# Optimization experiments

Hardware: AMD Instinct MI355X
Metric: run time of the kernel (lower is better)

## Reference

```python
import jax, jax.numpy as jnp
import numpy as np

N_TXN, N_CLI, N_E = 100000, 20000, 600000
D_TXN, D_CLI, H = 64, 32, 128


def setup_inputs() -> dict:
    key = jax.random.key(0)
    ks = jax.random.split(key, 24)
    s = 0.05
    inp = {
        'x_txn': jax.random.normal(ks[0], (N_TXN, D_TXN), jnp.float32),
        'x_client': jax.random.normal(ks[1], (N_CLI, D_CLI), jnp.float32),
        'ei_ct_src': jax.random.randint(ks[2], (N_E,), 0, N_CLI),
        'ei_ct_dst': jax.random.randint(ks[3], (N_E,), 0, N_TXN),
        'ei_tc_src': jax.random.randint(ks[4], (N_E,), 0, N_TXN),
        'ei_tc_dst': jax.random.randint(ks[5], (N_E,), 0, N_CLI),
        'W1_ct_l': jax.random.normal(ks[6], (D_CLI, H), jnp.float32) * s,
        'b1_ct': jnp.zeros((H,), jnp.float32),
        'W1_ct_r': jax.random.normal(ks[7], (D_TXN, H), jnp.float32) * s,
        'W1_tc_l': jax.random.normal(ks[8], (D_TXN, H), jnp.float32) * s,
        'b1_tc': jnp.zeros((H,), jnp.float32),
        'W1_tc_r': jax.random.normal(ks[9], (D_CLI, H), jnp.float32) * s,
        'W2_ct_l': jax.random.normal(ks[10], (H, H), jnp.float32) * s,
        'b2_ct': jnp.zeros((H,), jnp.float32),
        'W2_ct_r': jax.random.normal(ks[11], (H, H), jnp.float32) * s,
        'W2_tc_l': jax.random.normal(ks[12], (H, H), jnp.float32) * s,
        'b2_tc': jnp.zeros((H,), jnp.float32),
        'W2_tc_r': jax.random.normal(ks[13], (H, H), jnp.float32) * s,
        'Wd1': jax.random.normal(ks[14], (H, 64), jnp.float32) * s,
        'bd1': jnp.zeros((64,), jnp.float32),
        'Wd2': jax.random.normal(ks[15], (64, D_TXN), jnp.float32) * s,
        'bd2': jnp.zeros((D_TXN,), jnp.float32),
    }
    return inp


def _sage(x_src, x_dst, src, dst, Wl, bl, Wr, n_dst):
    # PyG SAGEConv: lin_l(mean_j x_src[j]) + lin_r(x_dst); lin_r has no bias.
    msg = x_src[src]                                             # [E, d_src]
    agg = jax.ops.segment_sum(msg, dst, num_segments=n_dst)     # [n_dst, d_src]
    cnt = jax.ops.segment_sum(jnp.ones((src.shape[0],), x_src.dtype), dst,
                              num_segments=n_dst)
    mean = agg / jnp.maximum(cnt, 1.0)[:, None]
    return mean @ Wl + bl + x_dst @ Wr


def reference(x_txn, x_client, ei_ct_src, ei_ct_dst, ei_tc_src, ei_tc_dst,
              W1_ct_l, b1_ct, W1_ct_r, W1_tc_l, b1_tc, W1_tc_r,
              W2_ct_l, b2_ct, W2_ct_r, W2_tc_l, b2_tc, W2_tc_r,
              Wd1, bd1, Wd2, bd2):
    # Layer 1 (hetero SAGEConv), then ReLU; dropout is identity in eval mode.
    h_txn = _sage(x_client, x_txn, ei_ct_src, ei_ct_dst, W1_ct_l, b1_ct, W1_ct_r, N_TXN)
    h_cli = _sage(x_txn, x_client, ei_tc_src, ei_tc_dst, W1_tc_l, b1_tc, W1_tc_r, N_CLI)
    h_txn = jax.nn.relu(h_txn)
    h_cli = jax.nn.relu(h_cli)
    # Layer 2
    z_txn = _sage(h_cli, h_txn, ei_ct_src, ei_ct_dst, W2_ct_l, b2_ct, W2_ct_r, N_TXN)
    z_cli = _sage(h_txn, h_cli, ei_tc_src, ei_tc_dst, W2_tc_l, b2_tc, W2_tc_r, N_CLI)
    # Decoder MLP on transaction embeddings
    recon = jax.nn.relu(z_txn @ Wd1 + bd1) @ Wd2 + bd2
    return (recon, z_txn, z_cli)
```

## Files before the change

### kernel.cpp

```cpp
#include <hip/hip_runtime.h>
#include <hip/hip_bf16.h>

typedef __hip_bfloat16 bf16;
typedef unsigned int uint;
typedef unsigned short ushort;
typedef __attribute__((ext_vector_type(8))) short short8;
typedef __attribute__((ext_vector_type(4))) float float4v;

__device__ __forceinline__ float lo2f(uint v) { return __uint_as_float(v << 16); }
__device__ __forceinline__ float hi2f(uint v) { return __uint_as_float(v & 0xffff0000u); }
__device__ __forceinline__ ushort f2bu(float v) {
  union { bf16 h; ushort u; } x;
  x.h = __float2bfloat16(v);
  return x.u;
}
__device__ __forceinline__ uint packbf2(float a, float b) {
  return (uint)f2bu(a) | ((uint)f2bu(b) << 16);
}

#define BSH 8
#define NBK_MAX 391

struct TJob { const float* wl; const float* wr; ushort* dst; int da, k, ncol, boff; };
struct TJobs { TJob j[6]; };

__global__ void transpose6_kernel(TJobs js) {
  int b = blockIdx.x;
  int jj = 0;
#pragma unroll
  for (int t = 1; t < 6; ++t)
    if (b >= js.j[t].boff) jj = t;
  const TJob J = js.j[jj];
  int i = (b - J.boff) * 256 + threadIdx.x;
  if (i >= J.k * J.ncol) return;
  int k = i / J.ncol, c = i - k * J.ncol;
  const float* srcp = (k < J.da) ? (J.wl + (long long)k * J.ncol)
                                 : (J.wr + (long long)(k - J.da) * J.ncol);
  J.dst[(long long)c * J.k + k] = f2bu(srcp[c]);
}

__global__ void bhist_kernel(const int* __restrict__ dA, int* __restrict__ cA, int nbkA,
                             const int* __restrict__ dB, int* __restrict__ cB, int nbkB,
                             int E, int chA) {
  __shared__ int h[NBK_MAX];
  int b = blockIdx.x;
  const int* dst; int* gc; int nbk;
  if (b < chA) { dst = dA; gc = cA; nbk = nbkA; }
  else         { b -= chA; dst = dB; gc = cB; nbk = nbkB; }
  for (int i = threadIdx.x; i < nbk; i += 256) h[i] = 0;
  __syncthreads();
  int e0 = b * 4096;
  for (int j = 0; j < 16; ++j) {
    int e = e0 + j * 256 + threadIdx.x;
    if (e < E) {
      uint B = (uint)dst[e] >> BSH;
      if (B < (uint)nbk) atomicAdd(&h[B], 1);
    }
  }
  __syncthreads();
  for (int i = threadIdx.x; i < nbk; i += 256)
    if (h[i]) atomicAdd(&gc[i], h[i]);
}

__global__ void bscan_kernel(const int* __restrict__ cA, int* __restrict__ oA,
                             int* __restrict__ uA, int nbkA,
                             const int* __restrict__ cB, int* __restrict__ oB,
                             int* __restrict__ uB, int nbkB) {
  __shared__ int s[512];
  const int* cnt; int* off; int* cur; int nbk;
  if (blockIdx.x == 0) { cnt = cA; off = oA; cur = uA; nbk = nbkA; }
  else                 { cnt = cB; off = oB; cur = uB; nbk = nbkB; }
  int t = threadIdx.x;
  int v = (t < nbk) ? cnt[t] : 0;
  s[t] = v;
  __syncthreads();
  for (int o = 1; o < 512; o <<= 1) {
    int x = (t >= o) ? s[t - o] : 0;
    __syncthreads();
    s[t] += x;
    __syncthreads();
  }
  if (t < nbk) { int ex = s[t] - v; off[t] = ex; cur[t] = ex; }
  if (t == nbk - 1) off[nbk] = s[t];
}

__global__ void multisplit_kernel(const int* __restrict__ sA, const int* __restrict__ dA,
                                  int* __restrict__ uA, uint2* __restrict__ seA, int nbkA,
                                  const int* __restrict__ sB, const int* __restrict__ dB,
                                  int* __restrict__ uB, uint2* __restrict__ seB, int nbkB,
                                  int E, int chA) {
  __shared__ int cnt[NBK_MAX];
  __shared__ int base[NBK_MAX];
  int b = blockIdx.x;
  const int *src, *dst; int* gcur; uint2* se; int nbk;
  if (b < chA) { src = sA; dst = dA; gcur = uA; se = seA; nbk = nbkA; }
  else         { b -= chA; src = sB; dst = dB; gcur = uB; se = seB; nbk = nbkB; }
  for (int i = threadIdx.x; i < nbk; i += 256) cnt[i] = 0;
  __syncthreads();
  int e0 = b * 4096;
  int mys[16], myd[16], myb[16], myr[16];
#pragma unroll
  for (int j = 0; j < 16; ++j) {
    int e = e0 + j * 256 + threadIdx.x;
    int s = 0, d = 0, bb = -1, r = 0;
    if (e < E) {
      s = src[e]; d = dst[e];
      uint B = (uint)d >> BSH;
      if (B < (uint)nbk) { bb = (int)B; r = atomicAdd(&cnt[bb], 1); }
    }
    mys[j] = s; myd[j] = d; myb[j] = bb; myr[j] = r;
  }
  __syncthreads();
  for (int i = threadIdx.x; i < nbk; i += 256) {
    int c = cnt[i];
    base[i] = c ? atomicAdd(&gcur[i], c) : 0;
  }
  __syncthreads();
#pragma unroll
  for (int j = 0; j < 16; ++j) {
    if (myb[j] >= 0) {
      uint2 v; v.x = (uint)mys[j]; v.y = (uint)myd[j];
      se[base[myb[j]] + myr[j]] = v;
    }
  }
}

__global__ void csr_fine_kernel(const uint2* __restrict__ seA, const int* __restrict__ boA,
                                int* __restrict__ offA, int* __restrict__ csrA, int nA, int nbkA,
                                const uint2* __restrict__ seB, const int* __restrict__ boB,
                                int* __restrict__ offB, int* __restrict__ csrB, int nB) {
  __shared__ int s[256];
  __shared__ int cur[256];
  int b = blockIdx.x;
  const uint2* se; const int* bo; int* off; int* csr; int n;
  if (b < nbkA) { se = seA; bo = boA; off = offA; csr = csrA; n = nA; }
  else          { b -= nbkA; se = seB; bo = boB; off = offB; csr = csrB; n = nB; }
  int t = threadIdx.x;
  int ebeg = bo[b], eend = bo[b + 1];
  cur[t] = 0;
  __syncthreads();
  for (int i = ebeg + t; i < eend; i += 256)
    atomicAdd(&cur[se[i].y & 255], 1);
  __syncthreads();
  int v = cur[t];
  s[t] = v;
  __syncthreads();
  for (int o = 1; o < 256; o <<= 1) {
    int x = (t >= o) ? s[t - o] : 0;
    __syncthreads();
    s[t] += x;
    __syncthreads();
  }
  int excl = s[t] - v;
  int node = b * 256 + t;
  if (node < n) off[node] = ebeg + excl;
  if (node == n - 1) off[n] = ebeg + excl + v;
  cur[t] = excl;
  __syncthreads();
  for (int i = ebeg + t; i < eend; i += 256) {
    uint2 e = se[i];
    int pos = ebeg + atomicAdd(&cur[e.y & 255], 1);
    csr[pos] = (int)e.x;
  }
}

__device__ __forceinline__ void acc8(float* a, uint4 v) {
  a[0] += lo2f(v.x); a[1] += hi2f(v.x);
  a[2] += lo2f(v.y); a[3] += hi2f(v.y);
  a[4] += lo2f(v.z); a[5] += hi2f(v.z);
  a[6] += lo2f(v.w); a[7] += hi2f(v.w);
}
__device__ __forceinline__ void acc4(float* a, float4 v) {
  a[0] += v.x; a[1] += v.y; a[2] += v.z; a[3] += v.w;
}

template <int D, bool XBF>
__device__ __forceinline__ void pull_worker(
    const int* __restrict__ off, const int* __restrict__ csr,
    const void* __restrict__ x, bf16* __restrict__ mean, int n, int nsrc,
    int blk0) {
  constexpr int EPL = XBF ? 8 : 4;
  constexpr int LPR = D / EPL;
  constexpr int PAR = 64 / LPR;
  int node = ((int)blockIdx.x - blk0) * 4 + (threadIdx.x >> 6);
  if (node >= n) return;
  int lane = threadIdx.x & 63;
  int h = lane / LPR, col = lane % LPR;
  int beg = off[node], deg = off[node + 1] - beg;
  float inv = 1.0f / fmaxf((float)deg, 1.0f);
  float a[EPL];
#pragma unroll
  for (int e = 0; e < EPL; ++e) a[e] = 0.f;

  int i = h;
  for (; i + 3 * PAR < deg; i += 4 * PAR) {
    int s0 = csr[beg + i];
    int s1 = csr[beg + i + PAR];
    int s2 = csr[beg + i + 2 * PAR];
    int s3 = csr[beg + i + 3 * PAR];
    s0 = ((unsigned)s0 < (unsigned)nsrc) ? s0 : 0;
    s1 = ((unsigned)s1 < (unsigned)nsrc) ? s1 : 0;
    s2 = ((unsigned)s2 < (unsigned)nsrc) ? s2 : 0;
    s3 = ((unsigned)s3 < (unsigned)nsrc) ? s3 : 0;
    if (XBF) {
      uint4 v0 = ((const uint4*)x)[(long long)s0 * LPR + col];
      uint4 v1 = ((const uint4*)x)[(long long)s1 * LPR + col];
      uint4 v2 = ((const uint4*)x)[(long long)s2 * LPR + col];
      uint4 v3 = ((const uint4*)x)[(long long)s3 * LPR + col];
      acc8(a, v0); acc8(a, v1); acc8(a, v2); acc8(a, v3);
    } else {
      float4 v0 = ((const float4*)x)[(long long)s0 * LPR + col];
      float4 v1 = ((const float4*)x)[(long long)s1 * LPR + col];
      float4 v2 = ((const float4*)x)[(long long)s2 * LPR + col];
      float4 v3 = ((const float4*)x)[(long long)s3 * LPR + col];
      acc4(a, v0); acc4(a, v1); acc4(a, v2); acc4(a, v3);
    }
  }
  for (; i < deg; i += PAR) {
    int s = csr[beg + i];
    s = ((unsigned)s < (unsigned)nsrc) ? s : 0;
    if (XBF) {
      uint4 v = ((const uint4*)x)[(long long)s * LPR + col];
      acc8(a, v);
    } else {
      float4 v = ((const float4*)x)[(long long)s * LPR + col];
      acc4(a, v);
    }
  }

#pragma unroll
  for (int m = LPR; m < 64; m <<= 1) {
#pragma unroll
    for (int e = 0; e < EPL; ++e) a[e] += __shfl_xor(a[e], m);
  }
  if (h == 0) {
    if (XBF) {
      uint4 o4;
      o4.x = packbf2(a[0] * inv, a[1] * inv);
      o4.y = packbf2(a[2] * inv, a[3] * inv);
      o4.z = packbf2(a[4] * inv, a[5] * inv);
      o4.w = packbf2(a[6] * inv, a[7] * inv);
      ((uint4*)mean)[(long long)node * LPR + col] = o4;
    } else {
      uint2 o2;
      o2.x = packbf2(a[0] * inv, a[1] * inv);
      o2.y = packbf2(a[2] * inv, a[3] * inv);
      ((uint2*)mean)[(long long)node * LPR + col] = o2;
    }
  }
}

template <int DA, bool XA, int DB, bool XB>
__global__ __launch_bounds__(256) void pull2_kernel(
    const int* __restrict__ offA, const int* __restrict__ csrA,
    const void* __restrict__ xA, bf16* __restrict__ meanA, int nA, int nsrcA,
    const int* __restrict__ offB, const int* __restrict__ csrB,
    const void* __restrict__ xB, bf16* __restrict__ meanB, int nB, int nsrcB,
    int nblkA) {
  if ((int)blockIdx.x < nblkA)
    pull_worker<DA, XA>(offA, csrA, xA, meanA, nA, nsrcA, 0);
  else
    pull_worker<DB, XB>(offB, csrB, xB, meanB, nB, nsrcB, nblkA);
}

#define AT_BF16 0
#define AT_F32  1
template <int KT, int NCT, int K0T, int A0T, int A1T, bool OUTF32, int MT>
__global__ __launch_bounds__(256, 2) void gemm_kernel(
    const void* __restrict__ A0, int lda0,
    const void* __restrict__ A1, int lda1,
    const ushort* __restrict__ Wt, const float* __restrict__ bias,
    void* __restrict__ C, long long cbase, int ldc, int n, int relu) {
  constexpr int K = KT * 32;
  int tid = threadIdx.x;
  int wave = tid >> 6, lane = tid & 63;
  int p = lane & 15, q = lane >> 4;
  int rowbase = blockIdx.x * (64 * MT) + wave * (16 * MT);

  int rcl[MT];
#pragma unroll
  for (int m = 0; m < MT; ++m) rcl[m] = min(rowbase + m * 16 + p, n - 1);

  float4v acc[MT][NCT];
#pragma unroll
  for (int m = 0; m < MT; ++m)
#pragma unroll
    for (int t = 0; t < NCT; ++t) acc[m][t] = (float4v){0.f, 0.f, 0.f, 0.f};

#pragma unroll
  for (int kt = 0; kt < KT; ++kt) {
    const bool seg0 = (kt < K0T);
    const void* ab = seg0 ? A0 : A1;
    const int lda = seg0 ? lda0 : lda1;
    const int kof = (seg0 ? kt : (kt - K0T)) * 32;
    const int at = seg0 ? A0T : A1T;
    short8 af[MT];
#pragma unroll
    for (int m = 0; m < MT; ++m) {
      long long base = (long long)rcl[m] * lda + kof + q * 8;
      if (at == AT_BF16) {
        af[m] = *(const short8*)((const bf16*)ab + base);
      } else {
        const float* fb = (const float*)ab + base;
        float4 a = *(const float4*)fb;
        float4 b = *(const float4*)(fb + 4);
        short8 r;
        r[0] = (short)f2bu(a.x); r[1] = (short)f2bu(a.y);
        r[2] = (short)f2bu(a.z); r[3] = (short)f2bu(a.w);
        r[4] = (short)f2bu(b.x); r[5] = (short)f2bu(b.y);
        r[6] = (short)f2bu(b.z); r[7] = (short)f2bu(b.w);
        af[m] = r;
      }
    }
#pragma unroll
    for (int t = 0; t < NCT; ++t) {
      int c = t * 16 + p;
      short8 bfr = *(const short8*)(Wt + (long long)c * K + kt * 32 + q * 8);
#pragma unroll
      for (int m = 0; m < MT; ++m)
        acc[m][t] = __builtin_amdgcn_mfma_f32_16x16x32_bf16(af[m], bfr, acc[m][t], 0, 0, 0);
    }
  }

#pragma unroll
  for (int m = 0; m < MT; ++m) {
#pragma unroll
    for (int t = 0; t < NCT; ++t) {
      int c = t * 16 + p;
      float bv = bias[c];
#pragma unroll
      for (int r = 0; r < 4; ++r) {
        int row = rowbase + m * 16 + q * 4 + r;
        if (row < n) {
          float v = acc[m][t][r] + bv;
          if (relu) v = fmaxf(v, 0.f);
          long long idx = cbase + (long long)row * ldc + c;
          if (OUTF32) ((float*)C)[idx] = v;
          else        ((bf16*)C)[idx] = __float2bfloat16(v);
        }
      }
    }
  }
}

__global__ __launch_bounds__(256, 2) void gemm_fused_dec_kernel(
    const bf16* __restrict__ A0,
    const bf16* __restrict__ A1,
    const ushort* __restrict__ W3,
    const float* __restrict__ b2,
    const ushort* __restrict__ W5,
    const float* __restrict__ bd1v,
    const ushort* __restrict__ W6,
    const float* __restrict__ bd2v,
    float* __restrict__ zout,
    float* __restrict__ recon,
    int n) {
  __shared__ __align__(16) char zls[65536];
  int tid = threadIdx.x;
  int wave = tid >> 6, lane = tid & 63;
  int p = lane & 15, q = lane >> 4;
  int rowbase = blockIdx.x * 256 + wave * 64;
  char* wls = zls + wave * 16384;
  const int sw = (p & 7) << 4;

  int rcl[4];
#pragma unroll
  for (int m = 0; m < 4; ++m) rcl[m] = min(rowbase + m * 16 + p, n - 1);

  float4v accz[4][8];
#pragma unroll
  for (int m = 0; m < 4; ++m)
#pragma unroll
    for (int t = 0; t < 8; ++t) accz[m][t] = (float4v){0.f, 0.f, 0.f, 0.f};

#pragma unroll
  for (int kt = 0; kt < 8; ++kt) {
    const bf16* ab = (kt < 4) ? A0 : A1;
    const int kof = (kt & 3) * 32;
    short8 af[4];
#pragma unroll
    for (int m = 0; m < 4; ++m)
      af[m] = *(const short8*)(ab + (long long)rcl[m] * 128 + kof + q * 8);
#pragma unroll
    for (int t = 0; t < 8; ++t) {
      short8 bfr = *(const short8*)(W3 + (long long)(t * 16 + p) * 256 + kt * 32 + q * 8);
#pragma unroll
      for (int m = 0; m < 4; ++m)
        accz[m][t] = __builtin_amdgcn_mfma_f32_16x16x32_bf16(bfr, af[m], accz[m][t], 0, 0, 0);
    }
  }

#pragma unroll
  for (int m = 0; m < 4; ++m) {
    int lr = m * 16 + p;
    int row = rowbase + lr;
#pragma unroll
    for (int t = 0; t < 8; ++t) {
      float4v bz = *(const float4v*)(b2 + t * 16 + q * 4);
      float4v v;
#pragma unroll
      for (int r = 0; r < 4; ++r) v[r] = accz[m][t][r] + bz[r];
      if (row < n)
        *(float4v*)(zout + (long long)row * 128 + t * 16 + q * 4) = v;
      uint2 u;
      u.x = packbf2(v[0], v[1]);
      u.y = packbf2(v[2], v[3]);
      *(uint2*)(wls + (((lr * 256 + t * 32 + q * 8)) ^ sw)) = u;
    }
  }
  __syncthreads();

  float4v accd[4][4];
#pragma unroll
  for (int m = 0; m < 4; ++m)
#pragma unroll
    for (int t = 0; t < 4; ++t) accd[m][t] = (float4v){0.f, 0.f, 0.f, 0.f};

#pragma unroll
  for (int kt2 = 0; kt2 < 4; ++kt2) {
    short8 zf[4];
#pragma unroll
    for (int m = 0; m < 4; ++m)
      zf[m] = *(const short8*)(wls + (((m * 16 + p) * 256 + kt2 * 64 + q * 16) ^ sw));
#pragma unroll
    for (int t2 = 0; t2 < 4; ++t2) {
      short8 wf = *(const short8*)(W5 + (long long)(t2 * 16 + p) * 128 + kt2 * 32 + q * 8);
#pragma unroll
      for (int m = 0; m < 4; ++m)
        accd[m][t2] = __builtin_amdgcn_mfma_f32_16x16x32_bf16(wf, zf[m], accd[m][t2], 0, 0, 0);
    }
  }
  __syncthreads();

#pragma unroll
  for (int m = 0; m < 4; ++m) {
    int lr = m * 16 + p;
#pragma unroll
    for (int t2 = 0; t2 < 4; ++t2) {
      float4v bb = *(const float4v*)(bd1v + t2 * 16 + q * 4);
      float4v v;
#pragma unroll
      for (int r = 0; r < 4; ++r) v[r] = fmaxf(accd[m][t2][r] + bb[r], 0.f);
      uint2 u;
      u.x = packbf2(v[0], v[1]);
      u.y = packbf2(v[2], v[3]);
      *(uint2*)(wls + (((lr * 128 + t2 * 32 + q * 8)) ^ sw)) = u;
    }
  }

  float4v accr[4][4];
#pragma unroll
  for (int m = 0; m < 4; ++m)
#pragma unroll
    for (int t = 0; t < 4; ++t) accr[m][t] = (float4v){0.f, 0.f, 0.f, 0.f};

#pragma unroll
  for (int kt3 = 0; kt3 < 2; ++kt3) {
    short8 df[4];
#pragma unroll
    for (int m = 0; m < 4; ++m)
      df[m] = *(const short8*)(wls + (((m * 16 + p) * 128 + kt3 * 64 + q * 16) ^ sw));
#pragma unroll
    for (int t3 = 0; t3 < 4; ++t3) {
      short8 wf = *(const short8*)(W6 + (long long)(t3 * 16 + p) * 64 + kt3 * 32 + q * 8);
#pragma unroll
      for (int m = 0; m < 4; ++m)
        accr[m][t3] = __builtin_amdgcn_mfma_f32_16x16x32_bf16(wf, df[m], accr[m][t3], 0, 0, 0);
    }
  }

#pragma unroll
  for (int m = 0; m < 4; ++m) {
    int row = rowbase + m * 16 + p;
    if (row < n) {
#pragma unroll
      for (int t3 = 0; t3 < 4; ++t3) {
        float4v bb = *(const float4v*)(bd2v + t3 * 16 + q * 4);
        float4v v;
#pragma unroll
        for (int r = 0; r < 4; ++r) v[r] = accr[m][t3][r] + bb[r];
        *(float4v*)(recon + (long long)row * 64 + t3 * 16 + q * 4) = v;
      }
    }
  }
}

extern "C" void kernel_launch(void* const* d_in, const int* in_sizes, int n_in,
                              void* d_out, int out_size, void* d_ws,
                              size_t ws_size, hipStream_t stream) {
  const float* x_txn = (const float*)d_in[0];
  const float* x_cli = (const float*)d_in[1];
  const int* ct_src = (const int*)d_in[2];
  const int* ct_dst = (const int*)d_in[3];
  const int* tc_src = (const int*)d_in[4];
  const int* tc_dst = (const int*)d_in[5];
  const float* W1ctl = (const float*)d_in[6];
  const float* b1ct  = (const float*)d_in[7];
  const float* W1ctr = (const float*)d_in[8];
  const float* W1tcl = (const float*)d_in[9];
  const float* b1tc  = (const float*)d_in[10];
  const float* W1tcr = (const float*)d_in[11];
  const float* W2ctl = (const float*)d_in[12];
  const float* b2ct  = (const float*)d_in[13];
  const float* W2ctr = (const float*)d_in[14];
  const float* W2tcl = (const float*)d_in[15];
  const float* b2tc  = (const float*)d_in[16];
  const float* W2tcr = (const float*)d_in[17];
  const float* Wd1   = (const float*)d_in[18];
  const float* bd1   = (const float*)d_in[19];
  const float* Wd2   = (const float*)d_in[20];
  const float* bd2   = (const float*)d_in[21];

  const int E = in_sizes[2];
  const int NT = 100000, NC = 20000;
  const int NBK_CT = (NT + 255) >> 8;
  const int NBK_TC = (NC + 255) >> 8;

  size_t o = 0;
  auto carve = [&](size_t bytes) {
    void* p = (char*)d_ws + o;
    o = (o + bytes + 255) & ~(size_t)255;
    return p;
  };
  int* bcnt_ct = (int*)carve((size_t)NBK_CT * 4);
  int* bcnt_tc = (int*)carve((size_t)NBK_TC * 4);
  size_t zero_bytes = o;
  int* boff_ct = (int*)carve((size_t)(NBK_CT + 1) * 4);
  int* boff_tc = (int*)carve((size_t)(NBK_TC + 1) * 4);
  int* bcur_ct = (int*)carve((size_t)NBK_CT * 4);
  int* bcur_tc = (int*)carve((size_t)NBK_TC * 4);
  uint2* se_ct = (uint2*)carve((size_t)E * 8);
  uint2* se_tc = (uint2*)carve((size_t)E * 8);
  int* off_ct = (int*)carve((size_t)(NT + 1) * 4);
  int* off_tc = (int*)carve((size_t)(NC + 1) * 4);
  int* csr_ct = (int*)carve((size_t)E * 4);
  int* csr_tc = (int*)carve((size_t)E * 4);
  ushort* Wt1 = (ushort*)carve((size_t)96 * 128 * 2);
  ushort* Wt2 = (ushort*)carve((size_t)96 * 128 * 2);
  ushort* Wt3 = (ushort*)carve((size_t)256 * 128 * 2);
  ushort* Wt4 = (ushort*)carve((size_t)256 * 128 * 2);
  ushort* Wt5 = (ushort*)carve((size_t)128 * 64 * 2);
  ushort* Wt6 = (ushort*)carve((size_t)64 * 64 * 2);
  bf16* mean1_ct = (bf16*)carve((size_t)NT * 32 * 2);
  bf16* mean1_tc = (bf16*)carve((size_t)NC * 64 * 2);
  bf16* h_txn    = (bf16*)carve((size_t)NT * 128 * 2);
  bf16* h_cli    = (bf16*)carve((size_t)NC * 128 * 2);
  bf16* mean2_ct = (bf16*)carve((size_t)NT * 128 * 2);
  bf16* mean2_tc = (bf16*)carve((size_t)NC * 128 * 2);
  (void)ws_size;

  hipMemsetAsync(d_ws, 0, zero_bytes, stream);

  const int tb = 256;
  const int CH = (E + 4095) / 4096;

  {
    TJobs js;
    auto blocks = [](int k, int ncol) { return (k * ncol + 255) / 256; };
    int boff = 0;
    auto setj = [&](int idx, const float* wl, const float* wr, ushort* dst,
                    int da, int k, int ncol) {
      js.j[idx] = TJob{wl, wr, dst, da, k, ncol, boff};
      boff += blocks(k, ncol);
    };
    setj(0, W1ctl, W1ctr, Wt1, 32, 96, 128);
    setj(1, W1tcl, W1tcr, Wt2, 64, 96, 128);
    setj(2, W2ctl, W2ctr, Wt3, 128, 256, 128);
    setj(3, W2tcl, W2tcr, Wt4, 128, 256, 128);
    setj(4, Wd1, Wd1, Wt5, 128, 128, 64);
    setj(5, Wd2, Wd2, Wt6, 64, 64, 64);
    transpose6_kernel<<<boff, tb, 0, stream>>>(js);
  }

  bhist_kernel<<<2 * CH, tb, 0, stream>>>(ct_dst, bcnt_ct, NBK_CT,
                                          tc_dst, bcnt_tc, NBK_TC, E, CH);
  bscan_kernel<<<2, 512, 0, stream>>>(bcnt_ct, boff_ct, bcur_ct, NBK_CT,
                                      bcnt_tc, boff_tc, bcur_tc, NBK_TC);
  multisplit_kernel<<<2 * CH, tb, 0, stream>>>(
      ct_src, ct_dst, bcur_ct, se_ct, NBK_CT,
      tc_src, tc_dst, bcur_tc, se_tc, NBK_TC, E, CH);
  csr_fine_kernel<<<NBK_CT + NBK_TC, tb, 0, stream>>>(
      se_ct, boff_ct, off_ct, csr_ct, NT, NBK_CT,
      se_tc, boff_tc, off_tc, csr_tc, NC);

  auto gbm = [](int n, int mt) { return (n + 64 * mt - 1) / (64 * mt); };
  const int pbA = (NT + 3) / 4, pbB = (NC + 3) / 4;

  pull2_kernel<32, false, 64, false><<<pbA + pbB, tb, 0, stream>>>(
      off_ct, csr_ct, x_cli, mean1_ct, NT, NC,
      off_tc, csr_tc, x_txn, mean1_tc, NC, NT, pbA);

  gemm_kernel<3, 8, 1, AT_BF16, AT_F32, false, 4><<<gbm(NT, 4), tb, 0, stream>>>(
      mean1_ct, 32, x_txn, 64, Wt1, b1ct, h_txn, 0, 128, NT, 1);
  gemm_kernel<3, 8, 2, AT_BF16, AT_F32, false, 1><<<gbm(NC, 1), tb, 0, stream>>>(
      mean1_tc, 64, x_cli, 32, Wt2, b1tc, h_cli, 0, 128, NC, 1);

  pull2_kernel<128, true, 128, true><<<pbA + pbB, tb, 0, stream>>>(
      off_ct, csr_ct, h_cli, mean2_ct, NT, NC,
      off_tc, csr_tc, h_txn, mean2_tc, NC, NT, pbA);

  float* out = (float*)d_out;
  const long long ztxn_base = (long long)NT * 64;
  const long long zcli_base = ztxn_base + (long long)NT * 128;

  gemm_fused_dec_kernel<<<gbm(NT, 4), tb, 0, stream>>>(
      mean2_ct, h_txn, Wt3, b2ct, Wt5, bd1, Wt6, bd2,
      out + ztxn_base, out, NT);

  gemm_kernel<8, 8, 4, AT_BF16, AT_BF16, true, 1><<<gbm(NC, 1), tb, 0, stream>>>(
      mean2_tc, 128, h_cli, 128, Wt4, b2tc, out, zcli_base, 128, NC, 0);
}
```

Baseline: 376.6 us.

## Fuse txn-side neighbor mean aggregation into both layer GEMM kernels via LDS

The client-to-transaction mean aggregation is moved into the GEMM kernels for both layers. Each wave gathers its 64 rows' neighbor sums into swizzled LDS and feeds them straight to MFMA, so the mean1_ct and mean2_ct intermediates are never written to or read back from global memory. The combined pull kernels become client-only pull kernels. The cost is that gather latency now sits inside GEMM blocks with lower occupancy, and the layer-1 kernel converts fp32 x_txn to bf16 on the fly.

```diff
diff --git a/kernel.cpp b/kernel.cpp
--- a/kernel.cpp
+++ b/kernel.cpp
@@ -250,17 +250,11 @@
   }
 }
 
-template <int DA, bool XA, int DB, bool XB>
-__global__ __launch_bounds__(256) void pull2_kernel(
-    const int* __restrict__ offA, const int* __restrict__ csrA,
-    const void* __restrict__ xA, bf16* __restrict__ meanA, int nA, int nsrcA,
-    const int* __restrict__ offB, const int* __restrict__ csrB,
-    const void* __restrict__ xB, bf16* __restrict__ meanB, int nB, int nsrcB,
-    int nblkA) {
-  if ((int)blockIdx.x < nblkA)
-    pull_worker<DA, XA>(offA, csrA, xA, meanA, nA, nsrcA, 0);
-  else
-    pull_worker<DB, XB>(offB, csrB, xB, meanB, nB, nsrcB, nblkA);
+template <int D, bool XBF>
+__global__ __launch_bounds__(256) void pull1_kernel(
+    const int* __restrict__ off, const int* __restrict__ csr,
+    const void* __restrict__ x, bf16* __restrict__ mean, int n, int nsrc) {
+  pull_worker<D, XBF>(off, csr, x, mean, n, nsrc, 0);
 }
 
 #define AT_BF16 0
@@ -343,8 +337,109 @@
   }
 }
 
+__global__ __launch_bounds__(256, 2) void gemm1a_fused_kernel(
+    const int* __restrict__ off, const int* __restrict__ csr,
+    const float* __restrict__ xg,
+    const float* __restrict__ A1,
+    const ushort* __restrict__ Wt,
+    const float* __restrict__ bias,
+    bf16* __restrict__ C,
+    int n, int nsrc) {
+  __shared__ __align__(16) char mls[16384];
+  int tid = threadIdx.x, wave = tid >> 6, lane = tid & 63;
+  int p = lane & 15, q = lane >> 4;
+  int rowbase = blockIdx.x * 256 + wave * 64;
+  char* wls = mls + wave * 4096;
+
+  {
+    int g = lane >> 3, li = lane & 7;
+    for (int it = 0; it < 8; ++it) {
+      int lr = it * 8 + g;
+      int node = min(rowbase + lr, n - 1);
+      int beg = off[node], deg = off[node + 1] - beg;
+      float inv = 1.0f / fmaxf((float)deg, 1.0f);
+      float4 a0 = {0.f, 0.f, 0.f, 0.f}, a1 = {0.f, 0.f, 0.f, 0.f};
+      int j = 0;
+      for (; j + 1 < deg; j += 2) {
+        int s0 = csr[beg + j], s1 = csr[beg + j + 1];
+        s0 = ((unsigned)s0 < (unsigned)nsrc) ? s0 : 0;
+        s1 = ((unsigned)s1 < (unsigned)nsrc) ? s1 : 0;
+        float4 v0 = ((const float4*)xg)[(long long)s0 * 8 + li];
+        float4 v1 = ((const float4*)xg)[(long long)s1 * 8 + li];
+        a0.x += v0.x; a0.y += v0.y; a0.z += v0.z; a0.w += v0.w;
+        a1.x += v1.x; a1.y += v1.y; a1.z += v1.z; a1.w += v1.w;
+      }
+      if (j < deg) {
+        int s0 = csr[beg + j];
+        s0 = ((unsigned)s0 < (unsigned)nsrc) ? s0 : 0;
+        float4 v0 = ((const float4*)xg)[(long long)s0 * 8 + li];
+        a0.x += v0.x; a0.y += v0.y; a0.z += v0.z; a0.w += v0.w;
+      }
+      uint2 u;
+      u.x = packbf2((a0.x + a1.x) * inv, (a0.y + a1.y) * inv);
+      u.y = packbf2((a0.z + a1.z) * inv, (a0.w + a1.w) * inv);
+      *(uint2*)(wls + ((lr * 64 + li * 8) ^ ((lr & 3) << 4))) = u;
+    }
+  }
+
+  int rcl[4];
+#pragma unroll
+  for (int m = 0; m < 4; ++m) rcl[m] = min(rowbase + m * 16 + p, n - 1);
+
+  float4v acc[4][8];
+#pragma unroll
+  for (int m = 0; m < 4; ++m)
+#pragma unroll
+    for (int t = 0; t < 8; ++t) acc[m][t] = (float4v){0.f, 0.f, 0.f, 0.f};
+
+  const int sw1 = (p & 3) << 4;
+#pragma unroll
+  for (int kt = 0; kt < 3; ++kt) {
+    short8 af[4];
+#pragma unroll
+    for (int m = 0; m < 4; ++m) {
+      if (kt == 0) {
+        af[m] = *(const short8*)(wls + ((((m * 16 + p) * 64) + q * 16) ^ sw1));
+      } else {
+        const float* fb = A1 + (long long)rcl[m] * 64 + (kt - 1) * 32 + q * 8;
+        float4 a = *(const float4*)fb;
+        float4 b = *(const float4*)(fb + 4);
+        short8 r;
+        r[0] = (short)f2bu(a.x); r[1] = (short)f2bu(a.y);
+        r[2] = (short)f2bu(a.z); r[3] = (short)f2bu(a.w);
+        r[4] = (short)f2bu(b.x); r[5] = (short)f2bu(b.y);
+        r[6] = (short)f2bu(b.z); r[7] = (short)f2bu(b.w);
+        af[m] = r;
+      }
+    }
+#pragma unroll
+    for (int t = 0; t < 8; ++t) {
+      short8 bfr = *(const short8*)(Wt + (long long)(t * 16 + p) * 96 + kt * 32 + q * 8);
+#pragma unroll
+      for (int m = 0; m < 4; ++m)
+        acc[m][t] = __builtin_amdgcn_mfma_f32_16x16x32_bf16(af[m], bfr, acc[m][t], 0, 0, 0);
+    }
+  }
+
+#pragma unroll
+  for (int m = 0; m < 4; ++m) {
+#pragma unroll
+    for (int t = 0; t < 8; ++t) {
+      int c = t * 16 + p;
+      float bv = bias[c];
+#pragma unroll
+      for (int r = 0; r < 4; ++r) {
+        int row = rowbase + m * 16 + q * 4 + r;
+        if (row < n)
+          C[(long long)row * 128 + c] = __float2bfloat16(fmaxf(acc[m][t][r] + bv, 0.f));
+      }
+    }
+  }
+}
+
 __global__ __launch_bounds__(256, 2) void gemm_fused_dec_kernel(
-    const bf16* __restrict__ A0,
+    const int* __restrict__ off, const int* __restrict__ csr,
+    const bf16* __restrict__ xg,
     const bf16* __restrict__ A1,
     const ushort* __restrict__ W3,
     const float* __restrict__ b2,
@@ -354,7 +449,7 @@
     const float* __restrict__ bd2v,
     float* __restrict__ zout,
     float* __restrict__ recon,
-    int n) {
+    int n, int nsrc) {
   __shared__ __align__(16) char zls[65536];
   int tid = threadIdx.x;
   int wave = tid >> 6, lane = tid & 63;
@@ -363,6 +458,40 @@
   char* wls = zls + wave * 16384;
   const int sw = (p & 7) << 4;
 
+  {
+    int g = lane >> 4, li = lane & 15;
+    for (int it = 0; it < 16; ++it) {
+      int lr = it * 4 + g;
+      int node = min(rowbase + lr, n - 1);
+      int beg = off[node], deg = off[node + 1] - beg;
+      float inv = 1.0f / fmaxf((float)deg, 1.0f);
+      float a0[8], a1[8];
+#pragma unroll
+      for (int e = 0; e < 8; ++e) { a0[e] = 0.f; a1[e] = 0.f; }
+      int j = 0;
+      for (; j + 1 < deg; j += 2) {
+        int s0 = csr[beg + j], s1 = csr[beg + j + 1];
+        s0 = ((unsigned)s0 < (unsigned)nsrc) ? s0 : 0;
+        s1 = ((unsigned)s1 < (unsigned)nsrc) ? s1 : 0;
+        uint4 v0 = ((const uint4*)xg)[(long long)s0 * 16 + li];
+        uint4 v1 = ((const uint4*)xg)[(long long)s1 * 16 + li];
+        acc8(a0, v0); acc8(a1, v1);
+      }
+      if (j < deg) {
+        int s0 = csr[beg + j];
+        s0 = ((unsigned)s0 < (unsigned)nsrc) ? s0 : 0;
+        uint4 v0 = ((const uint4*)xg)[(long long)s0 * 16 + li];
+        acc8(a0, v0);
+      }
+      uint4 u;
+      u.x = packbf2((a0[0] + a1[0]) * inv, (a0[1] + a1[1]) * inv);
+      u.y = packbf2((a0[2] + a1[2]) * inv, (a0[3] + a1[3]) * inv);
+      u.z = packbf2((a0[4] + a1[4]) * inv, (a0[5] + a1[5]) * inv);
+      u.w = packbf2((a0[6] + a1[6]) * inv, (a0[7] + a1[7]) * inv);
+      *(uint4*)(wls + ((lr * 256 + li * 16) ^ ((lr & 7) << 4))) = u;
+    }
+  }
+
   int rcl[4];
 #pragma unroll
   for (int m = 0; m < 4; ++m) rcl[m] = min(rowbase + m * 16 + p, n - 1);
@@ -375,12 +504,15 @@
 
 #pragma unroll
   for (int kt = 0; kt < 8; ++kt) {
-    const bf16* ab = (kt < 4) ? A0 : A1;
-    const int kof = (kt & 3) * 32;
     short8 af[4];
 #pragma unroll
-    for (int m = 0; m < 4; ++m)
-      af[m] = *(const short8*)(ab + (long long)rcl[m] * 128 + kof + q * 8);
+    for (int m = 0; m < 4; ++m) {
+      if (kt < 4) {
+        af[m] = *(const short8*)(wls + ((((m * 16 + p) * 256) + kt * 64 + q * 16) ^ sw));
+      } else {
+        af[m] = *(const short8*)(A1 + (long long)rcl[m] * 128 + (kt - 4) * 32 + q * 8);
+      }
+    }
 #pragma unroll
     for (int t = 0; t < 8; ++t) {
       short8 bfr = *(const short8*)(W3 + (long long)(t * 16 + p) * 256 + kt * 32 + q * 8);
@@ -541,11 +673,9 @@
   ushort* Wt4 = (ushort*)carve((size_t)256 * 128 * 2);
   ushort* Wt5 = (ushort*)carve((size_t)128 * 64 * 2);
   ushort* Wt6 = (ushort*)carve((size_t)64 * 64 * 2);
-  bf16* mean1_ct = (bf16*)carve((size_t)NT * 32 * 2);
   bf16* mean1_tc = (bf16*)carve((size_t)NC * 64 * 2);
   bf16* h_txn    = (bf16*)carve((size_t)NT * 128 * 2);
   bf16* h_cli    = (bf16*)carve((size_t)NC * 128 * 2);
-  bf16* mean2_ct = (bf16*)carve((size_t)NT * 128 * 2);
   bf16* mean2_tc = (bf16*)carve((size_t)NC * 128 * 2);
   (void)ws_size;
 
@@ -583,30 +713,28 @@
       se_ct, boff_ct, off_ct, csr_ct, NT, NBK_CT,
       se_tc, boff_tc, off_tc, csr_tc, NC);
 
-  auto gbm = [](int n, int mt) { return (n + 64 * mt - 1) / (64 * mt); };
-  const int pbA = (NT + 3) / 4, pbB = (NC + 3) / 4;
-
-  pull2_kernel<32, false, 64, false><<<pbA + pbB, tb, 0, stream>>>(
-      off_ct, csr_ct, x_cli, mean1_ct, NT, NC,
-      off_tc, csr_tc, x_txn, mean1_tc, NC, NT, pbA);
-
-  gemm_kernel<3, 8, 1, AT_BF16, AT_F32, false, 4><<<gbm(NT, 4), tb, 0, stream>>>(
-      mean1_ct, 32, x_txn, 64, Wt1, b1ct, h_txn, 0, 128, NT, 1);
-  gemm_kernel<3, 8, 2, AT_BF16, AT_F32, false, 1><<<gbm(NC, 1), tb, 0, stream>>>(
+  const int gNT = (NT + 255) / 256;
+
+  pull1_kernel<64, false><<<(NC + 3) / 4, tb, 0, stream>>>(
+      off_tc, csr_tc, x_txn, mean1_tc, NC, NT);
+
+  gemm1a_fused_kernel<<<gNT, tb, 0, stream>>>(
+      off_ct, csr_ct, x_cli, x_txn, Wt1, b1ct, h_txn, NT, NC);
+
+  gemm_kernel<3, 8, 2, AT_BF16, AT_F32, false, 1><<<(NC + 63) / 64, tb, 0, stream>>>(
       mean1_tc, 64, x_cli, 32, Wt2, b1tc, h_cli, 0, 128, NC, 1);
 
-  pull2_kernel<128, true, 128, true><<<pbA + pbB, tb, 0, stream>>>(
-      off_ct, csr_ct, h_cli, mean2_ct, NT, NC,
-      off_tc, csr_tc, h_txn, mean2_tc, NC, NT, pbA);
+  pull1_kernel<128, true><<<(NC + 3) / 4, tb, 0, stream>>>(
+      off_tc, csr_tc, h_txn, mean2_tc, NC, NT);
 
   float* out = (float*)d_out;
   const long long ztxn_base = (long long)NT * 64;
   const long long zcli_base = ztxn_base + (long long)NT * 128;
 
-  gemm_fused_dec_kernel<<<gbm(NT, 4), tb, 0, stream>>>(
-      mean2_ct, h_txn, Wt3, b2ct, Wt5, bd1, Wt6, bd2,
-      out + ztxn_base, out, NT);
-
-  gemm_kernel<8, 8, 4, AT_BF16, AT_BF16, true, 1><<<gbm(NC, 1), tb, 0, stream>>>(
+  gemm_fused_dec_kernel<<<gNT, tb, 0, stream>>>(
+      off_ct, csr_ct, h_cli, h_txn, Wt3, b2ct, Wt5, bd1, Wt6, bd2,
+      out + ztxn_base, out, NT, NC);
+
+  gemm_kernel<8, 8, 4, AT_BF16, AT_BF16, true, 1><<<(NC + 63) / 64, tb, 0, stream>>>(
       mean2_tc, 128, h_cli, 128, Wt4, b2tc, out, zcli_base, 128, NC, 0);
 }
```

Result: slower. 401.1 us (+6.5%).
